# Kernel tuning notes

Hardware: AMD Instinct MI355X
Metric: run time of the kernel (lower is better)

The kernel has to match this reference:

```python
import jax, jax.numpy as jnp
import numpy as np

EPSILON = 0.05   # entropic regularization
MAX_ITER = 50    # Sinkhorn iterations
STAB = 1e-8      # denominator stabilizer


def setup_inputs() -> dict:
    key = jax.random.key(0)
    B, n, m = 64, 512, 512
    C = jax.random.uniform(key, (B, n, m), dtype=jnp.float32)
    return {"C": C}


def reference(C):
    B, n, m = C.shape
    a = jnp.full((B, n), 1.0 / n, dtype=C.dtype)
    b = jnp.full((B, m), 1.0 / m, dtype=C.dtype)
    K = jnp.exp(-C / EPSILON)                      # [B, n, m]
    u0 = jnp.full((B, n), 1.0 / n, dtype=C.dtype)
    v0 = jnp.zeros((B, m), dtype=C.dtype)

    def step(carry, _):
        u, _v = carry
        # v = b / (K^T u + eps); u = a / (K v + eps)
        v = b / (jnp.einsum('bnm,bn->bm', K, u) + STAB)
        u = a / (jnp.einsum('bnm,bm->bn', K, v) + STAB)
        return (u, v), None

    (u, v), _ = jax.lax.scan(step, (u0, v0), None, length=MAX_ITER)
    P = u[:, :, None] * K * v[:, None, :]          # [B, n, m]
    ot_loss = jnp.sum(P * C, axis=(1, 2))          # [B]
    return (P, ot_loss)
```

## Files before the change

kernel.cpp:

```cpp
#include <hip/hip_runtime.h>
#include <hip/hip_fp16.h>

#define OT_B 64
#define OT_N 512
#define OT_M 512
#define OT_ITERS 50
#define OT_STAB 1e-8f
#define OT_NWG 4
#define OT_ROWS 128
#define OT_T 1024
#define KLDS_BYTES (OT_ROWS * 128 * sizeof(uint2))

__device__ __forceinline__ void group_barrier(int* cnt, int target) {
    __syncthreads();
    if (threadIdx.x == 0) {
        __hip_atomic_fetch_add(cnt, 1, __ATOMIC_RELEASE, __HIP_MEMORY_SCOPE_AGENT);
        while (__hip_atomic_load(cnt, __ATOMIC_RELAXED, __HIP_MEMORY_SCOPE_AGENT) < target)
            __builtin_amdgcn_s_sleep(2);
        asm volatile("" ::: "memory");
    }
    __syncthreads();
}

__global__ __launch_bounds__(OT_T, 1) void ot_sinkhorn_lds(
        const float* __restrict__ Cg,
        float* __restrict__ Pout,
        float* __restrict__ lossOut,
        float* __restrict__ partial,
        int* __restrict__ counters)
{
    extern __shared__ __align__(16) unsigned char smem[];
    uint2* __restrict__ Klds = (uint2*)smem;
    __shared__ __align__(16) float4 sp4[OT_T];
    __shared__ __align__(16) float v_lds[OT_M];
    __shared__ float u_lds[OT_ROWS];

    const int b = blockIdx.x & (OT_B - 1);
    const int g = blockIdx.x >> 6;
    const int t = threadIdx.x;
    const int r0 = g * OT_ROWS;

    const size_t sliceOff = ((size_t)b * OT_N + r0) * OT_M;
    const float4* C4 = (const float4*)(Cg + sliceOff);
    float4* P4 = (float4*)(Pout + sliceOff);
    int* cnt = counters + b * 32;
    float* spf = (float*)sp4;

    if (t < OT_ROWS) u_lds[t] = 1.0f / OT_N;
    #pragma unroll
    for (int ch = 0; ch < 16; ++ch) {
        int idx = ch * OT_T + t;
        int r = idx >> 7, c4 = idx & 127;
        float4 c = C4[idx];
        __half2 h0 = __floats2half2_rn(__expf(-20.f * c.x), __expf(-20.f * c.y));
        __half2 h1 = __floats2half2_rn(__expf(-20.f * c.z), __expf(-20.f * c.w));
        uint2 w;
        w.x = *(unsigned*)&h0;
        w.y = *(unsigned*)&h1;
        Klds[r * 128 + (c4 ^ (r & 15))] = w;
    }
    __syncthreads();

    const int p1 = t & 127;
    const int q1 = t >> 7;
    const int r2 = t & 127;
    const int q2 = t >> 7;

    for (int it = 0; it < OT_ITERS; ++it) {
        float* buf = partial + ((size_t)(it & 1) * OT_B + b) * (OT_NWG * OT_M);

        float4 acc = {0.f, 0.f, 0.f, 0.f};
        #pragma unroll
        for (int i = 0; i < 16; ++i) {
            int r = q1 * 16 + i;
            uint2 k4 = Klds[r * 128 + (p1 ^ (r & 15))];
            float2 a  = __half22float2(*(__half2*)&k4.x);
            float2 b2 = __half22float2(*(__half2*)&k4.y);
            float uu = u_lds[r];
            acc.x += a.x * uu;  acc.y += a.y * uu;
            acc.z += b2.x * uu; acc.w += b2.y * uu;
        }
        sp4[t] = acc;
        __syncthreads();
        if (t < 128) {
            float4 s = sp4[t];
            #pragma unroll
            for (int w = 1; w < 8; ++w) {
                float4 x = sp4[w * 128 + t];
                s.x += x.x; s.y += x.y; s.z += x.z; s.w += x.w;
            }
            float* dst = &buf[g * OT_M + 4 * t];
            __hip_atomic_store(dst + 0, s.x, __ATOMIC_RELAXED, __HIP_MEMORY_SCOPE_AGENT);
            __hip_atomic_store(dst + 1, s.y, __ATOMIC_RELAXED, __HIP_MEMORY_SCOPE_AGENT);
            __hip_atomic_store(dst + 2, s.z, __ATOMIC_RELAXED, __HIP_MEMORY_SCOPE_AGENT);
            __hip_atomic_store(dst + 3, s.w, __ATOMIC_RELAXED, __HIP_MEMORY_SCOPE_AGENT);
        }

        group_barrier(cnt, OT_NWG * (it + 1));

        if (t < OT_M) {
            float s = OT_STAB;
            #pragma unroll
            for (int w = 0; w < OT_NWG; ++w)
                s += __hip_atomic_load(&buf[w * OT_M + t], __ATOMIC_RELAXED,
                                       __HIP_MEMORY_SCOPE_AGENT);
            v_lds[t] = (1.0f / OT_M) / s;
        }
        __syncthreads();

        {
            float a2 = 0.f;
            const float4* v4 = (const float4*)v_lds;
            #pragma unroll
            for (int i = 0; i < 16; ++i) {
                int pp = q2 * 16 + i;
                uint2 k4 = Klds[r2 * 128 + (pp ^ (r2 & 15))];
                float2 a  = __half22float2(*(__half2*)&k4.x);
                float2 b2 = __half22float2(*(__half2*)&k4.y);
                float4 vv = v4[pp];
                a2 += a.x * vv.x + a.y * vv.y + b2.x * vv.z + b2.y * vv.w;
            }
            spf[t] = a2;
        }
        __syncthreads();
        if (t < 128) {
            float s = 0.f;
            #pragma unroll
            for (int w = 0; w < 8; ++w) s += spf[w * 128 + t];
            u_lds[t] = (1.0f / OT_N) / (s + OT_STAB);
        }
        __syncthreads();
    }

    float lacc = 0.f;
    {
        const float4* v4 = (const float4*)v_lds;
        const float4 vv = v4[p1];
        #pragma unroll
        for (int i = 0; i < 16; ++i) {
            int r = q1 * 16 + i;
            uint2 k4 = Klds[r * 128 + (p1 ^ (r & 15))];
            float2 a  = __half22float2(*(__half2*)&k4.x);
            float2 b2 = __half22float2(*(__half2*)&k4.y);
            float uu = u_lds[r];
            int idx = r * 128 + p1;
            float4 c = C4[idx];
            float4 pv;
            pv.x = uu * a.x * vv.x;  pv.y = uu * a.y * vv.y;
            pv.z = uu * b2.x * vv.z; pv.w = uu * b2.y * vv.w;
            P4[idx] = pv;
            lacc += pv.x * c.x + pv.y * c.y + pv.z * c.z + pv.w * c.w;
        }
    }
    __syncthreads();
    spf[t] = lacc;
    __syncthreads();
    #pragma unroll
    for (int s = OT_T / 2; s >= 64; s >>= 1) {
        if (t < s) spf[t] += spf[t + s];
        __syncthreads();
    }
    if (t < 64) {
        float rsum = spf[t];
        #pragma unroll
        for (int off = 32; off >= 1; off >>= 1) rsum += __shfl_xor(rsum, off);
        if (t == 0) atomicAdd(&lossOut[b], rsum);
    }
}

extern "C" void kernel_launch(void* const* d_in, const int* in_sizes, int n_in,
                              void* d_out, int out_size, void* d_ws, size_t ws_size,
                              hipStream_t stream) {
    const float* C = (const float*)d_in[0];
    float* P = (float*)d_out;
    float* loss = (float*)d_out + (size_t)OT_B * OT_N * OT_M;

    size_t off = 0;
    float* partial = (float*)((char*)d_ws + off);
    off += (size_t)2 * OT_B * OT_NWG * OT_M * sizeof(float);
    int* counters = (int*)((char*)d_ws + off);

    hipMemsetAsync(counters, 0, (size_t)OT_B * 32 * sizeof(int), stream);
    hipMemsetAsync(loss, 0, (size_t)OT_B * sizeof(float), stream);

    hipFuncSetAttribute((const void*)ot_sinkhorn_lds,
                        hipFuncAttributeMaxDynamicSharedMemorySize, KLDS_BYTES);

    ot_sinkhorn_lds<<<OT_B * OT_NWG, OT_T, KLDS_BYTES, stream>>>(C, P, loss,
                                                                 partial, counters);
}
```

Measured before the change: 383.2 us.

## Process two batches per workgroup to hide cross-workgroup barrier latency

Each workgroup now holds 64-row K slices for two batches, 8 workgroups per batch instead of 4, with 256 workgroups in total. After each phase-1 partial sum it signals an arrival and then runs the other batch's work before waiting. This interleaving is meant to overlap the spin-wait on the inter-workgroup counter with useful compute. The split barrier also removes one syncthreads, and partials are stored and loaded as 64-bit atomics. In exchange, each v update now reduces 8 partials per batch, and the double-slice LDS footprint, about 145KB, must fit the per-workgroup LDS limit.

```diff
diff --git a/kernel.cpp b/kernel.cpp
--- a/kernel.cpp
+++ b/kernel.cpp
@@ -6,23 +6,14 @@
 #define OT_M 512
 #define OT_ITERS 50
 #define OT_STAB 1e-8f
-#define OT_NWG 4
-#define OT_ROWS 128
+#define OT_NWG 8
+#define OT_ROWS 64
 #define OT_T 1024
-#define KLDS_BYTES (OT_ROWS * 128 * sizeof(uint2))
-
-__device__ __forceinline__ void group_barrier(int* cnt, int target) {
-    __syncthreads();
-    if (threadIdx.x == 0) {
-        __hip_atomic_fetch_add(cnt, 1, __ATOMIC_RELEASE, __HIP_MEMORY_SCOPE_AGENT);
-        while (__hip_atomic_load(cnt, __ATOMIC_RELAXED, __HIP_MEMORY_SCOPE_AGENT) < target)
-            __builtin_amdgcn_s_sleep(2);
-        asm volatile("" ::: "memory");
-    }
-    __syncthreads();
-}
-
-__global__ __launch_bounds__(OT_T, 1) void ot_sinkhorn_lds(
+#define NPAIR 32
+#define KSLICE_U (OT_ROWS * 256)
+#define DYN_BYTES (2 * KSLICE_U * 4 + 16384)
+
+__global__ __launch_bounds__(OT_T, 4) void ot_sinkhorn_dual(
         const float* __restrict__ Cg,
         float* __restrict__ Pout,
         float* __restrict__ lossOut,
@@ -30,141 +21,178 @@
         int* __restrict__ counters)
 {
     extern __shared__ __align__(16) unsigned char smem[];
-    uint2* __restrict__ Klds = (uint2*)smem;
-    __shared__ __align__(16) float4 sp4[OT_T];
-    __shared__ __align__(16) float v_lds[OT_M];
-    __shared__ float u_lds[OT_ROWS];
-
-    const int b = blockIdx.x & (OT_B - 1);
-    const int g = blockIdx.x >> 6;
+    unsigned* __restrict__ Klds = (unsigned*)smem;
+    float* __restrict__ scrf = (float*)(smem + 2 * KSLICE_U * 4);
+    float2* __restrict__ scr2 = (float2*)scrf;
+    __shared__ float v_lds[2][OT_M];
+    __shared__ float u_lds[2][OT_ROWS];
+
+    const int n = blockIdx.x;
+    const int g = n >> 5;
+    const int p = n & 31;
     const int t = threadIdx.x;
-    const int r0 = g * OT_ROWS;
-
-    const size_t sliceOff = ((size_t)b * OT_N + r0) * OT_M;
-    const float4* C4 = (const float4*)(Cg + sliceOff);
-    float4* P4 = (float4*)(Pout + sliceOff);
-    int* cnt = counters + b * 32;
-    float* spf = (float*)sp4;
-
-    if (t < OT_ROWS) u_lds[t] = 1.0f / OT_N;
-    #pragma unroll
-    for (int ch = 0; ch < 16; ++ch) {
-        int idx = ch * OT_T + t;
-        int r = idx >> 7, c4 = idx & 127;
-        float4 c = C4[idx];
-        __half2 h0 = __floats2half2_rn(__expf(-20.f * c.x), __expf(-20.f * c.y));
-        __half2 h1 = __floats2half2_rn(__expf(-20.f * c.z), __expf(-20.f * c.w));
-        uint2 w;
-        w.x = *(unsigned*)&h0;
-        w.y = *(unsigned*)&h1;
-        Klds[r * 128 + (c4 ^ (r & 15))] = w;
+
+    const int batA = p, batB = p + NPAIR;
+    const size_t offA = ((size_t)batA * OT_N + g * OT_ROWS) * OT_M;
+    const size_t offB = ((size_t)batB * OT_N + g * OT_ROWS) * OT_M;
+    int* cntA = counters + batA * 32;
+    int* cntB = counters + batB * 32;
+
+    {
+        const float4* C4A = (const float4*)(Cg + offA);
+        const float4* C4B = (const float4*)(Cg + offB);
+        #pragma unroll
+        for (int s = 0; s < 2; ++s) {
+            const float4* C4 = s ? C4B : C4A;
+            unsigned* Ks = Klds + s * KSLICE_U;
+            #pragma unroll
+            for (int ch = 0; ch < 8; ++ch) {
+                int idx = ch * OT_T + t;
+                int r = idx >> 7, c4 = idx & 127;
+                float4 c = C4[idx];
+                __half2 h0 = __floats2half2_rn(__expf(-20.f * c.x), __expf(-20.f * c.y));
+                __half2 h1 = __floats2half2_rn(__expf(-20.f * c.z), __expf(-20.f * c.w));
+                int d0 = 2 * c4;
+                Ks[r * 256 + ((d0)     ^ (r & 31))] = *(unsigned*)&h0;
+                Ks[r * 256 + ((d0 + 1) ^ (r & 31))] = *(unsigned*)&h1;
+            }
+        }
+        if (t < OT_ROWS) { u_lds[0][t] = 1.f / OT_N; u_lds[1][t] = 1.f / OT_N; }
+        __syncthreads();
     }
-    __syncthreads();
-
-    const int p1 = t & 127;
-    const int q1 = t >> 7;
-    const int r2 = t & 127;
-    const int q2 = t >> 7;
-
-    for (int it = 0; it < OT_ITERS; ++it) {
-        float* buf = partial + ((size_t)(it & 1) * OT_B + b) * (OT_NWG * OT_M);
-
-        float4 acc = {0.f, 0.f, 0.f, 0.f};
+
+    auto ph1 = [&](int s, float* buf) {
+        const int d1 = t & 255, q1 = t >> 8;
+        const unsigned* Ks = Klds + s * KSLICE_U;
+        float2 acc = {0.f, 0.f};
         #pragma unroll
         for (int i = 0; i < 16; ++i) {
             int r = q1 * 16 + i;
-            uint2 k4 = Klds[r * 128 + (p1 ^ (r & 15))];
-            float2 a  = __half22float2(*(__half2*)&k4.x);
-            float2 b2 = __half22float2(*(__half2*)&k4.y);
-            float uu = u_lds[r];
-            acc.x += a.x * uu;  acc.y += a.y * uu;
-            acc.z += b2.x * uu; acc.w += b2.y * uu;
-        }
-        sp4[t] = acc;
-        __syncthreads();
-        if (t < 128) {
-            float4 s = sp4[t];
-            #pragma unroll
-            for (int w = 1; w < 8; ++w) {
-                float4 x = sp4[w * 128 + t];
-                s.x += x.x; s.y += x.y; s.z += x.z; s.w += x.w;
-            }
-            float* dst = &buf[g * OT_M + 4 * t];
-            __hip_atomic_store(dst + 0, s.x, __ATOMIC_RELAXED, __HIP_MEMORY_SCOPE_AGENT);
-            __hip_atomic_store(dst + 1, s.y, __ATOMIC_RELAXED, __HIP_MEMORY_SCOPE_AGENT);
-            __hip_atomic_store(dst + 2, s.z, __ATOMIC_RELAXED, __HIP_MEMORY_SCOPE_AGENT);
-            __hip_atomic_store(dst + 3, s.w, __ATOMIC_RELAXED, __HIP_MEMORY_SCOPE_AGENT);
-        }
-
-        group_barrier(cnt, OT_NWG * (it + 1));
-
+            unsigned kk = Ks[r * 256 + (d1 ^ (r & 31))];
+            float2 f = __half22float2(*(__half2*)&kk);
+            float uu = u_lds[s][r];
+            acc.x += f.x * uu; acc.y += f.y * uu;
+        }
+        scr2[t] = acc;
+        __syncthreads();
+        if (t < 256) {
+            float2 a = scr2[t], b2 = scr2[t + 256], c2 = scr2[t + 512], d2 = scr2[t + 768];
+            float2 o;
+            o.x = a.x + b2.x + c2.x + d2.x;
+            o.y = a.y + b2.y + c2.y + d2.y;
+            unsigned long long bits;
+            __builtin_memcpy(&bits, &o, 8);
+            __hip_atomic_store((unsigned long long*)(buf + g * OT_M) + t, bits,
+                               __ATOMIC_RELAXED, __HIP_MEMORY_SCOPE_AGENT);
+        }
+        __syncthreads();
+    };
+    auto arrive = [&](int* cnt) {
+        if (t == 0)
+            __hip_atomic_fetch_add(cnt, 1, __ATOMIC_RELEASE, __HIP_MEMORY_SCOPE_AGENT);
+    };
+    auto waitc = [&](int* cnt, int target) {
+        if (t == 0) {
+            while (__hip_atomic_load(cnt, __ATOMIC_RELAXED, __HIP_MEMORY_SCOPE_AGENT) < target)
+                __builtin_amdgcn_s_sleep(2);
+            asm volatile("" ::: "memory");
+        }
+        __syncthreads();
+    };
+    auto ph2a = [&](int s, const float* buf) {
+        #pragma unroll
+        for (int k = 0; k < 2; ++k) {
+            int e = k * OT_T + t;
+            unsigned long long bits = __hip_atomic_load(
+                (const unsigned long long*)buf + e,
+                __ATOMIC_RELAXED, __HIP_MEMORY_SCOPE_AGENT);
+            float2 f;
+            __builtin_memcpy(&f, &bits, 8);
+            scr2[e] = f;
+        }
+        __syncthreads();
         if (t < OT_M) {
-            float s = OT_STAB;
-            #pragma unroll
-            for (int w = 0; w < OT_NWG; ++w)
-                s += __hip_atomic_load(&buf[w * OT_M + t], __ATOMIC_RELAXED,
-                                       __HIP_MEMORY_SCOPE_AGENT);
-            v_lds[t] = (1.0f / OT_M) / s;
-        }
-        __syncthreads();
-
-        {
-            float a2 = 0.f;
-            const float4* v4 = (const float4*)v_lds;
-            #pragma unroll
-            for (int i = 0; i < 16; ++i) {
-                int pp = q2 * 16 + i;
-                uint2 k4 = Klds[r2 * 128 + (pp ^ (r2 & 15))];
-                float2 a  = __half22float2(*(__half2*)&k4.x);
-                float2 b2 = __half22float2(*(__half2*)&k4.y);
-                float4 vv = v4[pp];
-                a2 += a.x * vv.x + a.y * vv.y + b2.x * vv.z + b2.y * vv.w;
-            }
-            spf[t] = a2;
-        }
-        __syncthreads();
-        if (t < 128) {
-            float s = 0.f;
-            #pragma unroll
-            for (int w = 0; w < 8; ++w) s += spf[w * 128 + t];
-            u_lds[t] = (1.0f / OT_N) / (s + OT_STAB);
-        }
-        __syncthreads();
+            float ssum = OT_STAB;
+            #pragma unroll
+            for (int w = 0; w < OT_NWG; ++w) ssum += scrf[w * OT_M + t];
+            v_lds[s][t] = (1.0f / OT_M) / ssum;
+        }
+        __syncthreads();
+    };
+    auto ph2b = [&](int s) {
+        const int r2 = t & 63, q2 = t >> 6;
+        const unsigned* Ks = Klds + s * KSLICE_U;
+        float a2 = 0.f;
+        #pragma unroll
+        for (int i = 0; i < 16; ++i) {
+            int d = q2 * 16 + i;
+            unsigned kk = Ks[r2 * 256 + (d ^ (r2 & 31))];
+            float2 f = __half22float2(*(__half2*)&kk);
+            float2 vv = ((const float2*)v_lds[s])[d];
+            a2 += f.x * vv.x + f.y * vv.y;
+        }
+        scrf[t] = a2;
+        __syncthreads();
+        if (t < OT_ROWS) {
+            float ssum = 0.f;
+            #pragma unroll
+            for (int w = 0; w < 16; ++w) ssum += scrf[w * OT_ROWS + t];
+            u_lds[s][t] = (1.0f / OT_N) / (ssum + OT_STAB);
+        }
+        __syncthreads();
+    };
+
+    for (int it = 0; it < OT_ITERS; ++it) {
+        float* bufA = partial + ((size_t)(it & 1) * OT_B + batA) * (OT_NWG * OT_M);
+        float* bufB = partial + ((size_t)(it & 1) * OT_B + batB) * (OT_NWG * OT_M);
+        const int tgt = OT_NWG * (it + 1);
+
+        ph1(0, bufA); arrive(cntA);
+        ph1(1, bufB); arrive(cntB);
+        waitc(cntA, tgt);
+        ph2a(0, bufA); ph2b(0);
+        waitc(cntB, tgt);
+        ph2a(1, bufB); ph2b(1);
     }
 
-    float lacc = 0.f;
-    {
-        const float4* v4 = (const float4*)v_lds;
-        const float4 vv = v4[p1];
+    #pragma unroll
+    for (int s = 0; s < 2; ++s) {
+        const size_t soff = s ? offB : offA;
+        const int sbat = s ? batB : batA;
+        const int d1 = t & 255, q1 = t >> 8;
+        const float2* C2 = (const float2*)(Cg + soff);
+        float2* P2 = (float2*)(Pout + soff);
+        const unsigned* Ks = Klds + s * KSLICE_U;
+        const float2 vv = ((const float2*)v_lds[s])[d1];
+        float lacc = 0.f;
         #pragma unroll
         for (int i = 0; i < 16; ++i) {
             int r = q1 * 16 + i;
-            uint2 k4 = Klds[r * 128 + (p1 ^ (r & 15))];
-            float2 a  = __half22float2(*(__half2*)&k4.x);
-            float2 b2 = __half22float2(*(__half2*)&k4.y);
-            float uu = u_lds[r];
-            int idx = r * 128 + p1;
-            float4 c = C4[idx];
-            float4 pv;
-            pv.x = uu * a.x * vv.x;  pv.y = uu * a.y * vv.y;
-            pv.z = uu * b2.x * vv.z; pv.w = uu * b2.y * vv.w;
-            P4[idx] = pv;
-            lacc += pv.x * c.x + pv.y * c.y + pv.z * c.z + pv.w * c.w;
-        }
-    }
-    __syncthreads();
-    spf[t] = lacc;
-    __syncthreads();
-    #pragma unroll
-    for (int s = OT_T / 2; s >= 64; s >>= 1) {
-        if (t < s) spf[t] += spf[t + s];
-        __syncthreads();
-    }
-    if (t < 64) {
-        float rsum = spf[t];
-        #pragma unroll
-        for (int off = 32; off >= 1; off >>= 1) rsum += __shfl_xor(rsum, off);
-        if (t == 0) atomicAdd(&lossOut[b], rsum);
+            unsigned kk = Ks[r * 256 + (d1 ^ (r & 31))];
+            float2 f = __half22float2(*(__half2*)&kk);
+            float uu = u_lds[s][r];
+            int idx = r * 256 + d1;
+            float2 c = C2[idx];
+            float2 pv;
+            pv.x = uu * f.x * vv.x;
+            pv.y = uu * f.y * vv.y;
+            P2[idx] = pv;
+            lacc += pv.x * c.x + pv.y * c.y;
+        }
+        __syncthreads();
+        scrf[t] = lacc;
+        __syncthreads();
+        #pragma unroll
+        for (int sh = OT_T / 2; sh >= 64; sh >>= 1) {
+            if (t < sh) scrf[t] += scrf[t + sh];
+            __syncthreads();
+        }
+        if (t < 64) {
+            float rs = scrf[t];
+            #pragma unroll
+            for (int off = 32; off >= 1; off >>= 1) rs += __shfl_xor(rs, off);
+            if (t == 0) atomicAdd(&lossOut[sbat], rs);
+        }
     }
 }
 
@@ -183,9 +211,9 @@
     hipMemsetAsync(counters, 0, (size_t)OT_B * 32 * sizeof(int), stream);
     hipMemsetAsync(loss, 0, (size_t)OT_B * sizeof(float), stream);
 
-    hipFuncSetAttribute((const void*)ot_sinkhorn_lds,
-                        hipFuncAttributeMaxDynamicSharedMemorySize, KLDS_BYTES);
-
-    ot_sinkhorn_lds<<<OT_B * OT_NWG, OT_T, KLDS_BYTES, stream>>>(C, P, loss,
-                                                                 partial, counters);
+    hipFuncSetAttribute((const void*)ot_sinkhorn_dual,
+                        hipFuncAttributeMaxDynamicSharedMemorySize, DYN_BYTES);
+
+    ot_sinkhorn_dual<<<OT_NWG * NPAIR, OT_T, DYN_BYTES, stream>>>(C, P, loss,
+                                                                  partial, counters);
 }
```

Measured after the change: 526.4 us. 37.4% more time.
